# Optimization experiments

Hardware: AMD Instinct MI355X
Metric: run time of the kernel (lower is better)

Reference implementation:

```python
import jax, jax.numpy as jnp
import numpy as np

B, S, E = 4, 1024, 512
H = 8
HD = E // H
FF = 4 * E
EPS = 1e-5


def _xavier(key, shape):
    fan_out, fan_in = shape
    std = (2.0 / (fan_in + fan_out)) ** 0.5
    return jax.random.normal(key, shape, dtype=jnp.float32) * std


def setup_inputs() -> dict:
    key = jax.random.key(0)
    ks = jax.random.split(key, 6)
    return {
        "x": jax.random.normal(ks[0], (B, S, E), dtype=jnp.float32),
        "ln1_w": jnp.ones((E,), jnp.float32),
        "ln1_b": jnp.zeros((E,), jnp.float32),
        "qkv_w": _xavier(ks[1], (3 * E, E)),
        "qkv_b": jnp.zeros((3 * E,), jnp.float32),
        "out_w": _xavier(ks[2], (E, E)),
        "out_b": jnp.zeros((E,), jnp.float32),
        "ln2_w": jnp.ones((E,), jnp.float32),
        "ln2_b": jnp.zeros((E,), jnp.float32),
        "fc1_w": _xavier(ks[3], (FF, E)),
        "fc1_b": jnp.zeros((FF,), jnp.float32),
        "fc2_w": _xavier(ks[4], (E, FF)),
        "fc2_b": jnp.zeros((E,), jnp.float32),
    }


def _layernorm(x, w, b):
    mu = jnp.mean(x, -1, keepdims=True)
    var = jnp.mean((x - mu) ** 2, -1, keepdims=True)
    return (x - mu) * jax.lax.rsqrt(var + EPS) * w + b


def _attention(x, qkv_w, qkv_b, out_w, out_b):
    b, s, _ = x.shape
    qkv = x @ qkv_w.T + qkv_b                      # [b, s, 3E]
    q, k, v = jnp.split(qkv, 3, axis=-1)
    def heads(t):
        return t.reshape(b, s, H, HD).transpose(0, 2, 1, 3)  # [b, H, s, hd]
    q, k, v = heads(q), heads(k), heads(v)
    # k is REPLACED by mean of q over seq, broadcast back to full length
    k_mean = jnp.mean(q, axis=2, keepdims=True)    # [b, H, 1, hd]
    k_full = jnp.broadcast_to(k_mean, q.shape)     # [b, H, s, hd]
    scale = HD ** (-0.5)
    attn = jnp.einsum("bhqd,bhkd->bhqk", q, k_full) * scale  # [b, H, s, s]
    attn = jax.nn.softmax(attn, axis=-1)           # rows are constant -> uniform 1/s
    z = jnp.einsum("bhqk,bhkd->bhqd", attn, v)     # [b, H, s, hd]
    z = z.transpose(0, 2, 1, 3).reshape(b, s, H * HD)
    return z @ out_w.T + out_b


def _mlp(x, fc1_w, fc1_b, fc2_w, fc2_b):
    h = jax.nn.gelu(x @ fc1_w.T + fc1_b, approximate=False)
    return h @ fc2_w.T + fc2_b


def reference(x, ln1_w, ln1_b, qkv_w, qkv_b, out_w, out_b,
              ln2_w, ln2_b, fc1_w, fc1_b, fc2_w, fc2_b):
    h = x
    x = _layernorm(x, ln1_w, ln1_b)
    x = _attention(x, qkv_w, qkv_b, out_w, out_b)
    x = x + h
    h = x
    x = _layernorm(x, ln2_w, ln2_b)
    x = _mlp(x, fc1_w, fc1_b, fc2_w, fc2_b)
    return x + h
```

## Files before the change

kernel.cpp:

```cpp
#include <hip/hip_runtime.h>
#include <hip/hip_bf16.h>
#include <math.h>

#define EPSLN 1e-5f

typedef __attribute__((ext_vector_type(8))) short short8;
typedef __attribute__((ext_vector_type(4))) float f32x4;
typedef __attribute__((ext_vector_type(4))) unsigned short u16x4;

__device__ inline unsigned short f2bf(float f){
  unsigned int u = __float_as_uint(f);
  u += 0x7fffu + ((u >> 16) & 1u);
  return (unsigned short)(u >> 16);
}

__device__ inline float wredb(float v){
  #pragma unroll
  for(int o = 1; o < 64; o <<= 1) v += __shfl_xor(v, o, 64);
  return v;
}

__device__ inline float wred(float v){
  #pragma unroll
  for(int o = 32; o > 0; o >>= 1) v += __shfl_down(v, o, 64);
  return v;
}

__global__ __launch_bounds__(256) void prep(
    const float* __restrict__ x, const float* __restrict__ ln1w,
    const float* __restrict__ ln1b, const float* __restrict__ fc1w,
    const float* __restrict__ fc2w, float* __restrict__ part,
    unsigned short* __restrict__ w1b, unsigned short* __restrict__ w2b)
{
  __shared__ float red[4][512];
  const int tid = threadIdx.x;
  const int blk = blockIdx.x;
  if(blk < 256){
    const int lane = tid & 63, wv = tid >> 6;
    const int b = blk >> 6, local = blk & 63;
    const f32x4* wp = (const f32x4*)ln1w;
    const f32x4* bp = (const f32x4*)ln1b;
    f32x4 w1 = wp[lane * 2], w2 = wp[lane * 2 + 1];
    f32x4 b1 = bp[lane * 2], b2 = bp[lane * 2 + 1];
    f32x4 a1 = (f32x4)(0.f), a2 = (f32x4)(0.f);
    const int r0 = local * 16 + wv * 4;
    for(int i = 0; i < 4; i++){
      const size_t row = (size_t)b * 1024 + r0 + i;
      const f32x4* xr = (const f32x4*)(x + row * 512);
      f32x4 v1 = xr[lane * 2], v2 = xr[lane * 2 + 1];
      float s = v1[0]+v1[1]+v1[2]+v1[3] + v2[0]+v2[1]+v2[2]+v2[3];
      float q = v1[0]*v1[0]+v1[1]*v1[1]+v1[2]*v1[2]+v1[3]*v1[3]
              + v2[0]*v2[0]+v2[1]*v2[1]+v2[2]*v2[2]+v2[3]*v2[3];
      s = wredb(s); q = wredb(q);
      float mu = s * (1.f / 512.f);
      float rs = rsqrtf(q * (1.f / 512.f) - mu * mu + EPSLN);
      #pragma unroll
      for(int j = 0; j < 4; j++){
        a1[j] += (v1[j] - mu) * rs * w1[j] + b1[j];
        a2[j] += (v2[j] - mu) * rs * w2[j] + b2[j];
      }
    }
    #pragma unroll
    for(int j = 0; j < 4; j++){
      red[wv][lane * 8 + j]     = a1[j];
      red[wv][lane * 8 + 4 + j] = a2[j];
    }
    __syncthreads();
    #pragma unroll
    for(int c = tid; c < 512; c += 256)
      part[(size_t)blk * 512 + c] = red[0][c] + red[1][c] + red[2][c] + red[3][c];
  } else {
    const int w = blk - 256;
    const float* src = (w < 1024) ? fc1w : fc2w;
    unsigned short* dst = (w < 1024) ? w1b : w2b;
    const int off = ((w & 1023) << 10) + tid * 4;
    f32x4 v = *(const f32x4*)(src + off);
    u16x4 r;
    #pragma unroll
    for(int j = 0; j < 4; j++) r[j] = f2bf(v[j]);
    *(u16x4*)(dst + off) = r;
  }
}

__global__ __launch_bounds__(256) void colsum_matvec(
    const float* __restrict__ part, const float* __restrict__ qkvw,
    const float* __restrict__ qkvb, float* __restrict__ vmean)
{
  __shared__ float cs[512];
  const int tid = threadIdx.x, lane = tid & 63, wv = tid >> 6;
  const int b = blockIdx.x >> 5;
  const int nb = (blockIdx.x & 31) * 16;
  #pragma unroll
  for(int c = tid; c < 512; c += 256){
    float s = 0.f;
    const float* pp = part + (size_t)(b * 64) * 512 + c;
    #pragma unroll 8
    for(int p = 0; p < 64; p++) s += pp[(size_t)p * 512];
    cs[c] = s;
  }
  __syncthreads();
  const f32x4* c4 = (const f32x4*)cs;
  f32x4 v1 = c4[lane * 2], v2 = c4[lane * 2 + 1];
  #pragma unroll
  for(int o = 0; o < 4; o++){
    int n = nb + wv * 4 + o;
    const f32x4* wr = (const f32x4*)(qkvw + (size_t)(1024 + n) * 512);
    f32x4 w1 = wr[lane * 2], w2 = wr[lane * 2 + 1];
    float s = 0.f;
    #pragma unroll
    for(int i = 0; i < 4; i++) s += v1[i] * w1[i] + v2[i] * w2[i];
    s = wred(s);
    if(lane == 0) vmean[b * 512 + n] = s * (1.f / 1024.f) + qkvb[1024 + n];
  }
}

__global__ __launch_bounds__(256) void matvec512(
    const float* __restrict__ vec, const float* __restrict__ Wm,
    const float* __restrict__ bias, float* __restrict__ outv)
{
  int gw = blockIdx.x * 4 + (threadIdx.x >> 6);
  int lane = threadIdx.x & 63;
  int b = gw >> 9, n = gw & 511;
  const f32x4* vr = (const f32x4*)(vec + ((size_t)b << 9));
  const f32x4* wr = (const f32x4*)(Wm + ((size_t)n << 9));
  f32x4 v1 = vr[lane * 2], v2 = vr[lane * 2 + 1];
  f32x4 w1 = wr[lane * 2], w2 = wr[lane * 2 + 1];
  float s = 0.f;
  #pragma unroll
  for(int i = 0; i < 4; i++) s += v1[i] * w1[i] + v2[i] * w2[i];
  s = wred(s);
  if(lane == 0) outv[gw] = s + bias[n];
}

__global__ __launch_bounds__(256) void add_ln2(
    const float* __restrict__ x, const float* __restrict__ arow,
    const float* __restrict__ w, const float* __restrict__ bb,
    unsigned short* __restrict__ xl2)
{
  const int tid = threadIdx.x, lane = tid & 63, wv = tid >> 6;
  const size_t row = (size_t)blockIdx.x * 4 + wv;
  const int b = (int)(row >> 10);
  const f32x4* xr = (const f32x4*)(x + row * 512);
  const f32x4* ar = (const f32x4*)(arow + ((size_t)b << 9));
  f32x4 v1 = xr[lane * 2], v2 = xr[lane * 2 + 1];
  f32x4 r1 = ar[lane * 2], r2 = ar[lane * 2 + 1];
  #pragma unroll
  for(int j = 0; j < 4; j++){ v1[j] += r1[j]; v2[j] += r2[j]; }
  float s = v1[0]+v1[1]+v1[2]+v1[3] + v2[0]+v2[1]+v2[2]+v2[3];
  float q = v1[0]*v1[0]+v1[1]*v1[1]+v1[2]*v1[2]+v1[3]*v1[3]
          + v2[0]*v2[0]+v2[1]*v2[1]+v2[2]*v2[2]+v2[3]*v2[3];
  s = wredb(s); q = wredb(q);
  float mu = s * (1.f / 512.f);
  float rs = rsqrtf(q * (1.f / 512.f) - mu * mu + EPSLN);
  const f32x4* wp = (const f32x4*)w;
  const f32x4* bp = (const f32x4*)bb;
  f32x4 w1 = wp[lane * 2], w2 = wp[lane * 2 + 1];
  f32x4 b1 = bp[lane * 2], b2 = bp[lane * 2 + 1];
  u16x4 o1, o2;
  #pragma unroll
  for(int j = 0; j < 4; j++){
    o1[j] = f2bf((v1[j] - mu) * rs * w1[j] + b1[j]);
    o2[j] = f2bf((v2[j] - mu) * rs * w2[j] + b2[j]);
  }
  u16x4* op = (u16x4*)(xl2 + row * 512 + lane * 8);
  op[0] = o1; op[1] = o2;
}

__device__ inline void gld_lds16(const void* g, void* l){
  __builtin_amdgcn_global_load_lds(
      (const __attribute__((address_space(1))) void*)g,
      (__attribute__((address_space(3))) void*)l, 16, 0, 0);
}

template<int BM, int BN, int BK, int EPI>
__global__ __launch_bounds__(256, 2) void gemm_bt(
    const unsigned short* __restrict__ A, const unsigned short* __restrict__ W,
    const float* __restrict__ bias, const float* __restrict__ resx,
    const float* __restrict__ resrow, void* __restrict__ outp,
    int M, int N, int K)
{
  constexpr int MI = BM / 32, NI = BN / 32;
  constexpr int KS = BK / 32;
  constexpr int PA = BM * BK / 2048;
  constexpr int PB = BN * BK / 2048;
  constexpr int RPA = BM / 64, RPB = BN / 64;
  __shared__ __align__(16) unsigned short sA[2][BM * BK];
  __shared__ __align__(16) unsigned short sB[2][BN * BK];
  const int tid = threadIdx.x, lane = tid & 63, wv = tid >> 6;
  const int wm = wv >> 1, wn = wv & 1;
  const int m0 = blockIdx.x * BM, n0 = blockIdx.y * BN;

  f32x4 acc[MI][NI];
  #pragma unroll
  for(int i = 0; i < MI; i++)
    #pragma unroll
    for(int j = 0; j < NI; j++) acc[i][j] = (f32x4)(0.f);

  const int rowS = tid >> 2;
  const int colb = (tid & 3) * 16;

  auto stage = [&](int buf, int k0){
    #pragma unroll
    for(int p = 0; p < PA; p++){
      const int h = p / RPA, rb = (p % RPA) * 64;
      const char* g = (const char*)(A + (size_t)(m0 + rb + rowS) * K + k0 + h * 32) + colb;
      gld_lds16(g, (char*)sA[buf] + p * 4096 + tid * 16);
    }
    #pragma unroll
    for(int p = 0; p < PB; p++){
      const int h = p / RPB, rb = (p % RPB) * 64;
      const char* g = (const char*)(W + (size_t)(n0 + rb + rowS) * K + k0 + h * 32) + colb;
      gld_lds16(g, (char*)sB[buf] + p * 4096 + tid * 16);
    }
  };

  const int NT = K / BK;
  stage(0, 0);
  __syncthreads();
  int cur = 0;
  for(int t = 0; t < NT; ++t){
    if(t + 1 < NT) stage(cur ^ 1, (t + 1) * BK);
    short8 af[MI][KS], bfr[NI][KS];
    const int kof = (lane >> 4) * 8;
    #pragma unroll
    for(int mi = 0; mi < MI; mi++)
      #pragma unroll
      for(int ks = 0; ks < KS; ks++)
        af[mi][ks] = *(const short8*)(sA[cur] + ks * (BM * 32)
                       + (wm * (BM / 2) + mi * 16 + (lane & 15)) * 32 + kof);
    #pragma unroll
    for(int ni = 0; ni < NI; ni++)
      #pragma unroll
      for(int ks = 0; ks < KS; ks++)
        bfr[ni][ks] = *(const short8*)(sB[cur] + ks * (BN * 32)
                       + (wn * (BN / 2) + ni * 16 + (lane & 15)) * 32 + kof);
    #pragma unroll
    for(int mi = 0; mi < MI; mi++)
      #pragma unroll
      for(int ni = 0; ni < NI; ni++)
        #pragma unroll
        for(int ks = 0; ks < KS; ks++)
          acc[mi][ni] = __builtin_amdgcn_mfma_f32_16x16x32_bf16(af[mi][ks], bfr[ni][ks], acc[mi][ni], 0, 0, 0);
    __syncthreads();
    cur ^= 1;
  }

  const int r0 = m0 + wm * (BM / 2) + (lane >> 4) * 4;
  const int c0 = n0 + wn * (BN / 2) + (lane & 15);
  #pragma unroll
  for(int mi = 0; mi < MI; mi++)
    #pragma unroll
    for(int ni = 0; ni < NI; ni++){
      int cc = c0 + ni * 16;
      float bi = bias[cc];
      #pragma unroll
      for(int j = 0; j < 4; j++){
        int rr = r0 + mi * 16 + j;
        float v = acc[mi][ni][j] + bi;
        if constexpr(EPI == 0){
          float u = v + 0.044715f * v * v * v;
          float gl = v / (1.f + __expf(-1.5957691216f * u));
          ((unsigned short*)outp)[(size_t)rr * N + cc] = f2bf(gl);
        } else {
          v += resx[(size_t)rr * N + cc] + resrow[((rr >> 10) << 9) + cc];
          ((float*)outp)[(size_t)rr * N + cc] = v;
        }
      }
    }
}

extern "C" void kernel_launch(void* const* d_in, const int* in_sizes, int n_in,
                              void* d_out, int out_size, void* d_ws, size_t ws_size,
                              hipStream_t stream)
{
  (void)in_sizes; (void)n_in; (void)out_size; (void)ws_size;
  const float* x    = (const float*)d_in[0];
  const float* ln1w = (const float*)d_in[1];
  const float* ln1b = (const float*)d_in[2];
  const float* qkvw = (const float*)d_in[3];
  const float* qkvb = (const float*)d_in[4];
  const float* outw = (const float*)d_in[5];
  const float* outb = (const float*)d_in[6];
  const float* ln2w = (const float*)d_in[7];
  const float* ln2b = (const float*)d_in[8];
  const float* fc1w = (const float*)d_in[9];
  const float* fc1b = (const float*)d_in[10];
  const float* fc2w = (const float*)d_in[11];
  const float* fc2b = (const float*)d_in[12];

  char* ws = (char*)d_ws;
  float*          part   = (float*)ws;
  float*          vmean  = (float*)(ws + (1u << 19));
  float*          arow   = (float*)(ws + (1u << 19) + 8192);
  unsigned short* xl2    = (unsigned short*)(ws + (1u << 20));
  unsigned short* w1b    = (unsigned short*)(ws + (5u << 20));
  unsigned short* w2b    = (unsigned short*)(ws + (7u << 20));
  unsigned short* hact   = (unsigned short*)(ws + (9u << 20));

  prep<<<2304, 256, 0, stream>>>(x, ln1w, ln1b, fc1w, fc2w, part, w1b, w2b);
  colsum_matvec<<<128, 256, 0, stream>>>(part, qkvw, qkvb, vmean);
  matvec512<<<512, 256, 0, stream>>>(vmean, outw, outb, arow);
  add_ln2<<<1024, 256, 0, stream>>>(x, arow, ln2w, ln2b, xl2);
  gemm_bt<128, 128, 64, 0><<<dim3(32, 16), 256, 0, stream>>>(
      xl2, w1b, fc1b, nullptr, nullptr, hact, 4096, 2048, 512);
  gemm_bt<64, 64, 128, 1><<<dim3(64, 8), 256, 0, stream>>>(
      hact, w2b, fc2b, x, arow, d_out, 4096, 512, 2048);
}
```

Measured before the change: 63.04 us.

## Switch GEMM to 32x32x16 bf16 MFMA with fragment-ordered LDS staging

Replaces the 16x16x32 MFMA tiles with 32x32x16 MFMA, so each wave issues fewer, larger matrix instructions with 16-wide accumulators. The LDS staging layout is reorganised so every wave loads whole 32x16 fragment blocks that lanes can read contiguously. The epilogue is rewritten to match the 32x32 output fragment mapping. This aims to raise MFMA efficiency and simplify LDS reads, at the cost of more accumulator registers per wave and possible occupancy pressure.

```diff
diff --git a/kernel.cpp b/kernel.cpp
--- a/kernel.cpp
+++ b/kernel.cpp
@@ -6,6 +6,7 @@
 
 typedef __attribute__((ext_vector_type(8))) short short8;
 typedef __attribute__((ext_vector_type(4))) float f32x4;
+typedef __attribute__((ext_vector_type(16))) float f32x16;
 typedef __attribute__((ext_vector_type(4))) unsigned short u16x4;
 
 __device__ inline unsigned short f2bf(float f){
@@ -179,38 +180,41 @@
     const float* __restrict__ resrow, void* __restrict__ outp,
     int M, int N, int K)
 {
-  constexpr int MI = BM / 32, NI = BN / 32;
-  constexpr int KS = BK / 32;
-  constexpr int PA = BM * BK / 2048;
-  constexpr int PB = BN * BK / 2048;
-  constexpr int RPA = BM / 64, RPB = BN / 64;
+  constexpr int MI = BM / 64, NI = BN / 64;
+  constexpr int KS = BK / 16;
+  constexpr int FRA = BM / 32, FRB = BN / 32;
+  constexpr int NBA = KS * FRA;
+  constexpr int NBB = KS * FRB;
+  static_assert(NBA % 4 == 0 && NBB % 4 == 0, "waves stage whole blocks");
   __shared__ __align__(16) unsigned short sA[2][BM * BK];
   __shared__ __align__(16) unsigned short sB[2][BN * BK];
   const int tid = threadIdx.x, lane = tid & 63, wv = tid >> 6;
   const int wm = wv >> 1, wn = wv & 1;
   const int m0 = blockIdx.x * BM, n0 = blockIdx.y * BN;
-
-  f32x4 acc[MI][NI];
+  const int lrow = lane & 31, lkh = lane >> 5;
+
+  f32x16 acc[MI][NI];
   #pragma unroll
   for(int i = 0; i < MI; i++)
     #pragma unroll
-    for(int j = 0; j < NI; j++) acc[i][j] = (f32x4)(0.f);
-
-  const int rowS = tid >> 2;
-  const int colb = (tid & 3) * 16;
+    for(int j = 0; j < NI; j++) acc[i][j] = (f32x16)(0.f);
 
   auto stage = [&](int buf, int k0){
     #pragma unroll
-    for(int p = 0; p < PA; p++){
-      const int h = p / RPA, rb = (p % RPA) * 64;
-      const char* g = (const char*)(A + (size_t)(m0 + rb + rowS) * K + k0 + h * 32) + colb;
-      gld_lds16(g, (char*)sA[buf] + p * 4096 + tid * 16);
-    }
-    #pragma unroll
-    for(int p = 0; p < PB; p++){
-      const int h = p / RPB, rb = (p % RPB) * 64;
-      const char* g = (const char*)(W + (size_t)(n0 + rb + rowS) * K + k0 + h * 32) + colb;
-      gld_lds16(g, (char*)sB[buf] + p * 4096 + tid * 16);
+    for(int p = 0; p < NBA / 4; p++){
+      const int bi = wv * (NBA / 4) + p;
+      const int ks = bi / FRA, fr = bi % FRA;
+      const unsigned short* g = A + (size_t)(m0 + fr * 32 + lrow) * K
+                                  + k0 + ks * 16 + lkh * 8;
+      gld_lds16(g, (char*)sA[buf] + bi * 1024 + lane * 16);
+    }
+    #pragma unroll
+    for(int p = 0; p < NBB / 4; p++){
+      const int bi = wv * (NBB / 4) + p;
+      const int ks = bi / FRB, fr = bi % FRB;
+      const unsigned short* g = W + (size_t)(n0 + fr * 32 + lrow) * K
+                                  + k0 + ks * 16 + lkh * 8;
+      gld_lds16(g, (char*)sB[buf] + bi * 1024 + lane * 16);
     }
   };
 
@@ -221,42 +225,41 @@
   for(int t = 0; t < NT; ++t){
     if(t + 1 < NT) stage(cur ^ 1, (t + 1) * BK);
     short8 af[MI][KS], bfr[NI][KS];
-    const int kof = (lane >> 4) * 8;
-    #pragma unroll
-    for(int mi = 0; mi < MI; mi++)
-      #pragma unroll
-      for(int ks = 0; ks < KS; ks++)
-        af[mi][ks] = *(const short8*)(sA[cur] + ks * (BM * 32)
-                       + (wm * (BM / 2) + mi * 16 + (lane & 15)) * 32 + kof);
-    #pragma unroll
-    for(int ni = 0; ni < NI; ni++)
-      #pragma unroll
-      for(int ks = 0; ks < KS; ks++)
-        bfr[ni][ks] = *(const short8*)(sB[cur] + ks * (BN * 32)
-                       + (wn * (BN / 2) + ni * 16 + (lane & 15)) * 32 + kof);
+    #pragma unroll
+    for(int ks = 0; ks < KS; ks++)
+      #pragma unroll
+      for(int mi = 0; mi < MI; mi++)
+        af[mi][ks] = *(const short8*)(sA[cur]
+                       + (ks * FRA + wm * MI + mi) * 512 + lane * 8);
+    #pragma unroll
+    for(int ks = 0; ks < KS; ks++)
+      #pragma unroll
+      for(int ni = 0; ni < NI; ni++)
+        bfr[ni][ks] = *(const short8*)(sB[cur]
+                       + (ks * FRB + wn * NI + ni) * 512 + lane * 8);
     #pragma unroll
     for(int mi = 0; mi < MI; mi++)
       #pragma unroll
       for(int ni = 0; ni < NI; ni++)
         #pragma unroll
         for(int ks = 0; ks < KS; ks++)
-          acc[mi][ni] = __builtin_amdgcn_mfma_f32_16x16x32_bf16(af[mi][ks], bfr[ni][ks], acc[mi][ni], 0, 0, 0);
+          acc[mi][ni] = __builtin_amdgcn_mfma_f32_32x32x16_bf16(
+              af[mi][ks], bfr[ni][ks], acc[mi][ni], 0, 0, 0);
     __syncthreads();
     cur ^= 1;
   }
 
-  const int r0 = m0 + wm * (BM / 2) + (lane >> 4) * 4;
-  const int c0 = n0 + wn * (BN / 2) + (lane & 15);
   #pragma unroll
   for(int mi = 0; mi < MI; mi++)
     #pragma unroll
     for(int ni = 0; ni < NI; ni++){
-      int cc = c0 + ni * 16;
-      float bi = bias[cc];
-      #pragma unroll
-      for(int j = 0; j < 4; j++){
-        int rr = r0 + mi * 16 + j;
-        float v = acc[mi][ni][j] + bi;
+      const int cc = n0 + wn * (BN / 2) + ni * 32 + lrow;
+      const float bi = bias[cc];
+      #pragma unroll
+      for(int r = 0; r < 16; r++){
+        const int rr = m0 + wm * (BM / 2) + mi * 32
+                     + (r & 3) + 8 * (r >> 2) + 4 * lkh;
+        float v = acc[mi][ni][r] + bi;
         if constexpr(EPI == 0){
           float u = v + 0.044715f * v * v * v;
           float gl = v / (1.f + __expf(-1.5957691216f * u));
```

New measurement: 82.86 us. 31.4% more time.

## Load GEMM weight fragments directly from global into registers, bypassing LDS

Applied to the files above, without the earlier changes.

The weight (B) operand is no longer staged through shared memory. Each wave now reads its MFMA B fragments straight from global memory into two register buffers, and the main loop is unrolled by two to alternate them with the A LDS buffers. The goal is to cut LDS traffic and footprint and to drop the LDS read step for B. In exchange, the two waves sharing a column tile load the same data twice, global accesses are strided by K and less coalesced, and register pressure rises under the 2-blocks-per-SM launch bound. The unroll-by-two loop also assumes an even tile count along K.

```diff
diff --git a/kernel.cpp b/kernel.cpp
--- a/kernel.cpp
+++ b/kernel.cpp
@@ -182,10 +182,8 @@
   constexpr int MI = BM / 32, NI = BN / 32;
   constexpr int KS = BK / 32;
   constexpr int PA = BM * BK / 2048;
-  constexpr int PB = BN * BK / 2048;
-  constexpr int RPA = BM / 64, RPB = BN / 64;
+  constexpr int RPA = BM / 64;
   __shared__ __align__(16) unsigned short sA[2][BM * BK];
-  __shared__ __align__(16) unsigned short sB[2][BN * BK];
   const int tid = threadIdx.x, lane = tid & 63, wv = tid >> 6;
   const int wm = wv >> 1, wn = wv & 1;
   const int m0 = blockIdx.x * BM, n0 = blockIdx.y * BN;
@@ -198,51 +196,57 @@
 
   const int rowS = tid >> 2;
   const int colb = (tid & 3) * 16;
-
-  auto stage = [&](int buf, int k0){
+  const int kof  = (lane >> 4) * 8;
+
+  const unsigned short* Wl = W + (size_t)(n0 + wn * (BN / 2) + (lane & 15)) * K + kof;
+
+  auto stageA = [&](int buf, int k0){
     #pragma unroll
     for(int p = 0; p < PA; p++){
       const int h = p / RPA, rb = (p % RPA) * 64;
       const char* g = (const char*)(A + (size_t)(m0 + rb + rowS) * K + k0 + h * 32) + colb;
       gld_lds16(g, (char*)sA[buf] + p * 4096 + tid * 16);
     }
-    #pragma unroll
-    for(int p = 0; p < PB; p++){
-      const int h = p / RPB, rb = (p % RPB) * 64;
-      const char* g = (const char*)(W + (size_t)(n0 + rb + rowS) * K + k0 + h * 32) + colb;
-      gld_lds16(g, (char*)sB[buf] + p * 4096 + tid * 16);
-    }
   };
 
-  const int NT = K / BK;
-  stage(0, 0);
-  __syncthreads();
-  int cur = 0;
-  for(int t = 0; t < NT; ++t){
-    if(t + 1 < NT) stage(cur ^ 1, (t + 1) * BK);
-    short8 af[MI][KS], bfr[NI][KS];
-    const int kof = (lane >> 4) * 8;
+  auto loadB = [&](short8 (&br)[NI][KS], int k0){
+    #pragma unroll
+    for(int ni = 0; ni < NI; ni++)
+      #pragma unroll
+      for(int ks = 0; ks < KS; ks++)
+        br[ni][ks] = *(const short8*)(Wl + (size_t)ni * 16 * K + k0 + ks * 32);
+  };
+
+  auto compute = [&](const unsigned short* sAc, short8 (&br)[NI][KS]){
+    short8 af[MI][KS];
     #pragma unroll
     for(int mi = 0; mi < MI; mi++)
       #pragma unroll
       for(int ks = 0; ks < KS; ks++)
-        af[mi][ks] = *(const short8*)(sA[cur] + ks * (BM * 32)
+        af[mi][ks] = *(const short8*)(sAc + ks * (BM * 32)
                        + (wm * (BM / 2) + mi * 16 + (lane & 15)) * 32 + kof);
-    #pragma unroll
-    for(int ni = 0; ni < NI; ni++)
-      #pragma unroll
-      for(int ks = 0; ks < KS; ks++)
-        bfr[ni][ks] = *(const short8*)(sB[cur] + ks * (BN * 32)
-                       + (wn * (BN / 2) + ni * 16 + (lane & 15)) * 32 + kof);
     #pragma unroll
     for(int mi = 0; mi < MI; mi++)
       #pragma unroll
       for(int ni = 0; ni < NI; ni++)
         #pragma unroll
         for(int ks = 0; ks < KS; ks++)
-          acc[mi][ni] = __builtin_amdgcn_mfma_f32_16x16x32_bf16(af[mi][ks], bfr[ni][ks], acc[mi][ni], 0, 0, 0);
+          acc[mi][ni] = __builtin_amdgcn_mfma_f32_16x16x32_bf16(
+              af[mi][ks], br[ni][ks], acc[mi][ni], 0, 0, 0);
+  };
+
+  const int NT = K / BK;
+  short8 b0[NI][KS], b1[NI][KS];
+  stageA(0, 0);
+  loadB(b0, 0);
+  __syncthreads();
+  for(int t = 0; t < NT; t += 2){
+    if(t + 1 < NT){ stageA(1, (t + 1) * BK); loadB(b1, (t + 1) * BK); }
+    compute(sA[0], b0);
     __syncthreads();
-    cur ^= 1;
+    if(t + 2 < NT){ stageA(0, (t + 2) * BK); loadB(b0, (t + 2) * BK); }
+    compute(sA[1], b1);
+    __syncthreads();
   }
 
   const int r0 = m0 + wm * (BM / 2) + (lane >> 4) * 4;
```

New measurement: 88.77 us. 1.41x slower.
